# Kernel optimization log

Measured on AMD Instinct MI355X. Metric: run time of the kernel, lower is better.

## Reference

```python
import jax, jax.numpy as jnp
import numpy as np

NUM_EXPERTS = 3
INPUT_DIM = 1024
HIDDEN_DIM = 4096
OUTPUT_DIM = 1024
ROUTER_HIDDEN = 128
BATCH = 8192


def setup_inputs() -> dict:
    key = jax.random.key(0)
    ks = jax.random.split(key, 6)
    s_in = 1.0 / np.sqrt(INPUT_DIM)
    s_h = 1.0 / np.sqrt(HIDDEN_DIM)
    s_rh = 1.0 / np.sqrt(ROUTER_HIDDEN)
    return {
        "x": jax.random.normal(ks[0], (BATCH, INPUT_DIM), jnp.float32),
        "router_w1": jax.random.normal(ks[1], (INPUT_DIM, ROUTER_HIDDEN), jnp.float32) * s_in,
        "router_b1": jnp.zeros((ROUTER_HIDDEN,), jnp.float32),
        "router_w2": jax.random.normal(ks[2], (ROUTER_HIDDEN, NUM_EXPERTS), jnp.float32) * s_rh,
        "router_b2": jnp.zeros((NUM_EXPERTS,), jnp.float32),
        "expert_w1": jax.random.normal(ks[3], (NUM_EXPERTS, INPUT_DIM, HIDDEN_DIM), jnp.float32) * s_in,
        "expert_b1": jnp.zeros((NUM_EXPERTS, HIDDEN_DIM), jnp.float32),
        "expert_w2": jax.random.normal(ks[4], (NUM_EXPERTS, HIDDEN_DIM, OUTPUT_DIM), jnp.float32) * s_h,
        "expert_b2": jnp.zeros((NUM_EXPERTS, OUTPUT_DIM), jnp.float32),
    }


def reference(x, router_w1, router_b1, router_w2, router_b2,
              expert_w1, expert_b1, expert_w2, expert_b2):
    # Router: MLP -> softmax probs, hard top-1 selection (argmax)
    rh = jax.nn.relu(x @ router_w1 + router_b1)          # [B, 128]
    logits = rh @ router_w2 + router_b2                   # [B, E]
    probs = jax.nn.softmax(logits, axis=-1)
    selected = jnp.argmax(probs, axis=-1)                 # [B] int

    # Per-expert forward on all tokens (dense equivalent of masked dispatch)
    h = jax.nn.relu(jnp.einsum('bi,eih->ebh', x, expert_w1) + expert_b1[:, None, :])  # [E,B,H]
    y = jnp.einsum('ebh,eho->ebo', h, expert_w2) + expert_b2[:, None, :]              # [E,B,O]

    # Scatter-combine: each token takes its selected expert's output
    outputs = jnp.take_along_axis(
        y, selected[None, :, None], axis=0)[0]            # [B, O]

    # routing_stats: tokens per expert
    routing_stats = jnp.bincount(selected, length=NUM_EXPERTS)
    return outputs, routing_stats
```

## Files before the change

### kernel.cpp

```cpp
#include <hip/hip_runtime.h>
#include <hip/hip_bf16.h>

typedef short bf16x8 __attribute__((ext_vector_type(8)));
typedef float f32x4 __attribute__((ext_vector_type(4)));
typedef __attribute__((address_space(1))) const void gconst_t;
typedef __attribute__((address_space(3))) void lds_t;

#define DEVI __device__ __forceinline__

constexpr int BATCH   = 8192;
constexpr int IN_DIM  = 1024;
constexpr int HID     = 4096;
constexpr int OUT_DIM = 1024;
constexpr int NE      = 3;

constexpr size_t XBF_OFF  = 0;
constexpr size_t W1T_OFF  = 16777216;
constexpr size_t W2T_OFF  = W1T_OFF + 25165824;
constexpr size_t H_OFF    = W2T_OFF + 25165824;
constexpr size_t XLO_OFF  = H_OFF;
constexpr size_t RHP_OFF  = H_OFF + 16777216;
constexpr size_t META_OFF = H_OFF + 67108864;
constexpr size_t W3_OFF   = META_OFF + 131072;

DEVI unsigned short f2bf(float f) {
  __hip_bfloat16 h = __float2bfloat16(f);
  return *reinterpret_cast<unsigned short*>(&h);
}
DEVI float bf2f(unsigned short u) {
  unsigned v = (unsigned)u << 16;
  return __uint_as_float(v);
}

DEVI unsigned swz(unsigned b) { return b ^ (((b >> 7) & 7u) << 4); }

__global__ __launch_bounds__(256) void prepA_kernel(
    const float* __restrict__ x, const float* __restrict__ rw1,
    unsigned short* __restrict__ xb, unsigned short* __restrict__ xlo,
    unsigned short* __restrict__ w3) {
  __shared__ float tile[64][65];
  const int b = blockIdx.x;
  const int tid = threadIdx.x;
  if (b < 512) {
    const float4* xv4 = (const float4*)x;
    const int total = BATCH * IN_DIM / 4;
    for (int i = b * 256 + tid; i < total; i += 512 * 256) {
      const float4 v = xv4[i];
      ushort4 h, l;
      h.x = f2bf(v.x); l.x = f2bf(v.x - bf2f(h.x));
      h.y = f2bf(v.y); l.y = f2bf(v.y - bf2f(h.y));
      h.z = f2bf(v.z); l.z = f2bf(v.z - bf2f(h.z));
      h.w = f2bf(v.w); l.w = f2bf(v.w - bf2f(h.w));
      ((ushort4*)xb)[i] = h;
      ((ushort4*)xlo)[i] = l;
    }
  } else {
    const int w = b - 512;
    const int r0 = (w >> 1) * 64;
    const int c0 = (w & 1) * 64;
    const int tr = tid >> 4;
    const int tc = (tid & 15) << 2;
#pragma unroll
    for (int i = 0; i < 4; i++) {
      const int r = tr + i * 16;
      const float4 v = *(const float4*)(rw1 + (size_t)(r0 + r) * 128 + (c0 + tc));
      tile[r][tc + 0] = v.x; tile[r][tc + 1] = v.y; tile[r][tc + 2] = v.z; tile[r][tc + 3] = v.w;
    }
    __syncthreads();
#pragma unroll
    for (int i = 0; i < 4; i++) {
      const int c = tr + i * 16;
      ushort4 hi, lo;
      {
        float f;
        f = tile[tc + 0][c]; hi.x = f2bf(f); lo.x = f2bf(f - bf2f(hi.x));
        f = tile[tc + 1][c]; hi.y = f2bf(f); lo.y = f2bf(f - bf2f(hi.y));
        f = tile[tc + 2][c]; hi.z = f2bf(f); lo.z = f2bf(f - bf2f(hi.z));
        f = tile[tc + 3][c]; hi.w = f2bf(f); lo.w = f2bf(f - bf2f(hi.w));
      }
      unsigned short* base = w3 + (size_t)(c0 + c) * 3072 + (r0 + tc);
      *(ushort4*)(base)        = hi;
      *(ushort4*)(base + 1024) = hi;
      *(ushort4*)(base + 2048) = lo;
    }
  }
}

__global__ __launch_bounds__(256) void router_part(
    const unsigned short* __restrict__ xhi, const unsigned short* __restrict__ xlo,
    const unsigned short* __restrict__ w3, float* __restrict__ rhpart) {
  __shared__ unsigned short At[128 * 64];
  __shared__ unsigned short Bt[128 * 64];
  const int tid = threadIdx.x;
  const int m0 = blockIdx.x * 128;
  const int seg = blockIdx.y;
  const unsigned short* Abase = (seg == 1) ? xlo : xhi;
  const int kcol0 = seg * 1024;

  const unsigned short* asrc[4];
  const unsigned short* bsrc[4];
  unsigned loff[4];
#pragma unroll
  for (int l = 0; l < 4; l++) {
    const unsigned o = l * 4096u + (unsigned)tid * 16u;
    const unsigned p = swz(o);
    const int row = (int)(o >> 7);
    const int kel = (int)((p & 127u) >> 1);
    loff[l] = o;
    asrc[l] = Abase + (size_t)(m0 + row) * 1024 + kel;
    bsrc[l] = w3 + (size_t)row * 3072 + kcol0 + kel;
  }

  f32x4 acc[4][4];
#pragma unroll
  for (int i = 0; i < 4; i++)
#pragma unroll
    for (int j = 0; j < 4; j++) acc[i][j] = {0.f, 0.f, 0.f, 0.f};

  const int lane = tid & 63;
  const int wave = tid >> 6;
  const int wm = (wave >> 1) * 64;
  const int wn = (wave & 1) * 64;
  const int fr = lane & 15;
  const int fc = lane >> 4;

  for (int t = 0; t < 16; ++t) {
    __syncthreads();
#pragma unroll
    for (int l = 0; l < 4; l++) {
      __builtin_amdgcn_global_load_lds((gconst_t*)(asrc[l] + t * 64),
                                       (lds_t*)((char*)At + loff[l]), 16, 0, 0);
      __builtin_amdgcn_global_load_lds((gconst_t*)(bsrc[l] + t * 64),
                                       (lds_t*)((char*)Bt + loff[l]), 16, 0, 0);
    }
    __syncthreads();
    bf16x8 af[2][4], bv[2][4];
#pragma unroll
    for (int ks = 0; ks < 2; ks++) {
#pragma unroll
      for (int m = 0; m < 4; m++) {
        const unsigned L = (unsigned)(wm + m * 16 + fr) * 128u + (unsigned)(ks * 64 + fc * 16);
        af[ks][m] = *(const bf16x8*)((const char*)At + swz(L));
      }
#pragma unroll
      for (int n = 0; n < 4; n++) {
        const unsigned L = (unsigned)(wn + n * 16 + fr) * 128u + (unsigned)(ks * 64 + fc * 16);
        bv[ks][n] = *(const bf16x8*)((const char*)Bt + swz(L));
      }
    }
#pragma unroll
    for (int ks = 0; ks < 2; ks++)
#pragma unroll
      for (int m = 0; m < 4; m++)
#pragma unroll
        for (int n = 0; n < 4; n++)
          acc[m][n] = __builtin_amdgcn_mfma_f32_16x16x32_bf16(af[ks][m], bv[ks][n], acc[m][n], 0, 0, 0);
  }

  const int crow = (lane >> 4) * 4;
  const int ccol = lane & 15;
  float* outp = rhpart + (size_t)seg * BATCH * 128;
#pragma unroll
  for (int mi = 0; mi < 4; mi++) {
#pragma unroll
    for (int r = 0; r < 4; r++) {
      const int tok = m0 + wm + mi * 16 + crow + r;
#pragma unroll
      for (int ni = 0; ni < 4; ni++)
        outp[(size_t)tok * 128 + (wn + ni * 16 + ccol)] = acc[mi][ni][r];
    }
  }
}

__global__ __launch_bounds__(256) void router_finish(
    const float* __restrict__ rhpart, const float* __restrict__ rb1,
    const float* __restrict__ rw2, const float* __restrict__ rb2,
    int* __restrict__ counts, int* __restrict__ toklist) {
  __shared__ float rh[128 * 132];
  __shared__ float lg[128 * 3];
  const int tid = threadIdx.x;
  const int t0 = blockIdx.x * 128;
  constexpr size_t SEG = (size_t)BATCH * 128;

  for (int i = tid; i < 128 * 32; i += 256) {
    const int tok = i >> 5;
    const int c4 = (i & 31) * 4;
    const size_t base = (size_t)(t0 + tok) * 128 + c4;
    const float4 a = *(const float4*)(rhpart + base);
    const float4 b = *(const float4*)(rhpart + SEG + base);
    const float4 c = *(const float4*)(rhpart + 2 * SEG + base);
    const float4 bb = *(const float4*)(rb1 + c4);
    rh[tok * 132 + c4 + 0] = fmaxf(a.x + b.x + c.x + bb.x, 0.f);
    rh[tok * 132 + c4 + 1] = fmaxf(a.y + b.y + c.y + bb.y, 0.f);
    rh[tok * 132 + c4 + 2] = fmaxf(a.z + b.z + c.z + bb.z, 0.f);
    rh[tok * 132 + c4 + 3] = fmaxf(a.w + b.w + c.w + bb.w, 0.f);
  }
  __syncthreads();
#pragma unroll
  for (int pass = 0; pass < 2; ++pass) {
    const int t = tid + pass * 256;
    if (t < 384) {
      const int tok = t / 3, e = t - tok * 3;
      float s = rb2[e];
#pragma unroll 4
      for (int j = 0; j < 128; ++j) s = fmaf(rh[tok * 132 + j], rw2[j * 3 + e], s);
      lg[tok * 3 + e] = s;
    }
  }
  __syncthreads();
  if (tid < 128) {
    const float l0 = lg[tid * 3], l1 = lg[tid * 3 + 1], l2 = lg[tid * 3 + 2];
    int sel = 0; float m = l0;
    if (l1 > m) { m = l1; sel = 1; }
    if (l2 > m) { m = l2; sel = 2; }
    const int slot = atomicAdd(&counts[sel], 1);
    toklist[sel * BATCH + slot] = t0 + tid;
  }
}

__global__ __launch_bounds__(256) void prep2_kernel(
    const float* __restrict__ ew1, const float* __restrict__ ew2,
    unsigned short* __restrict__ w1t, unsigned short* __restrict__ w2t) {
  __shared__ float tile[64][65];
  const int b = blockIdx.x;
  const int tid = threadIdx.x;

  const float* src; unsigned short* dst; int R, C, r0, c0;
  if (b < 3072) {
    const int e = b / 1024, w = b % 1024;
    src = ew1 + (size_t)e * 1024 * 4096; dst = w1t + (size_t)e * 4096 * 1024;
    R = 1024; C = 4096; r0 = (w & 15) * 64; c0 = (w >> 4) * 64;
  } else {
    const int bb = b - 3072, e = bb / 1024, w = bb % 1024;
    src = ew2 + (size_t)e * 4096 * 1024; dst = w2t + (size_t)e * 1024 * 4096;
    R = 4096; C = 1024; r0 = (w & 63) * 64; c0 = (w >> 6) * 64;
  }
  const int tr = tid >> 4;
  const int tc = (tid & 15) << 2;
#pragma unroll
  for (int i = 0; i < 4; i++) {
    const int r = tr + i * 16;
    const float4 v = *(const float4*)(src + (size_t)(r0 + r) * C + (c0 + tc));
    tile[r][tc + 0] = v.x; tile[r][tc + 1] = v.y; tile[r][tc + 2] = v.z; tile[r][tc + 3] = v.w;
  }
  __syncthreads();
#pragma unroll
  for (int i = 0; i < 4; i++) {
    const int c = tr + i * 16;
    ushort4 o;
    o.x = f2bf(tile[tc + 0][c]);
    o.y = f2bf(tile[tc + 1][c]);
    o.z = f2bf(tile[tc + 2][c]);
    o.w = f2bf(tile[tc + 3][c]);
    *(ushort4*)(dst + (size_t)(c0 + c) * R + (r0 + tc)) = o;
  }
}

template <int MODE>
__global__ __launch_bounds__(512, 2) void moe_gemm(
    const unsigned short* __restrict__ Abase, const unsigned short* __restrict__ Ball,
    const float* __restrict__ biasAll, unsigned short* __restrict__ Hout,
    float* __restrict__ Yout, const int* __restrict__ toklist, const int* __restrict__ counts,
    float* __restrict__ tail) {
  constexpr int N  = (MODE == 0) ? HID : OUT_DIM;
  constexpr int K  = (MODE == 0) ? IN_DIM : HID;
  constexpr int NT = K / 32;

  const int tid = threadIdx.x;
  if (MODE == 0 && blockIdx.x == 0 && blockIdx.y == 0 && tid < NE)
    tail[tid] = (float)counts[tid];

  const int c0 = counts[0], c1 = counts[1], c2 = counts[2];
  const int mb0 = (c0 + 127) >> 7, mb1 = (c1 + 127) >> 7, mb2 = (c2 + 127) >> 7;
  const int bx = blockIdx.x;
  int e, mblk;
  if (bx < mb0) { e = 0; mblk = bx; }
  else if (bx < mb0 + mb1) { e = 1; mblk = bx - mb0; }
  else if (bx < mb0 + mb1 + mb2) { e = 2; mblk = bx - mb0 - mb1; }
  else return;
  const int cnt = (e == 0) ? c0 : (e == 1) ? c1 : c2;
  const int m0 = mblk * 128;
  const int n0 = blockIdx.y * 256;
  const int off_e = (e > 0 ? c0 : 0) + (e > 1 ? c1 : 0);
  const unsigned short* Bmat = Ball + (size_t)e * ((size_t)N * K);
  const float* bias = biasAll + (size_t)e * N;

  __shared__ unsigned short Ab[3][128 * 32];
  __shared__ unsigned short Bb[3][256 * 32];

  const unsigned short* asrc;
  const unsigned short* bsrc[2];
  unsigned aoff, boff[2];
  {
    const unsigned o = (unsigned)tid * 16u;
    const unsigned p = o ^ (((o >> 6) & 3u) << 4);
    const int row = (int)(o >> 6);
    const int kel = (int)((p & 63u) >> 1);
    aoff = o;
    int slot = m0 + row; if (slot > cnt - 1) slot = cnt - 1;
    const size_t arow = (MODE == 0) ? (size_t)toklist[e * BATCH + slot]
                                    : (size_t)(off_e + slot);
    asrc = Abase + arow * K + kel;
  }
#pragma unroll
  for (int l = 0; l < 2; l++) {
    const unsigned o = l * 8192u + (unsigned)tid * 16u;
    const unsigned p = o ^ (((o >> 6) & 3u) << 4);
    const int row = (int)(o >> 6);
    const int kel = (int)((p & 63u) >> 1);
    boff[l] = o;
    bsrc[l] = Bmat + (size_t)(n0 + row) * K + kel;
  }

  f32x4 acc[4][4];
#pragma unroll
  for (int i = 0; i < 4; i++)
#pragma unroll
    for (int j = 0; j < 4; j++) acc[i][j] = {0.f, 0.f, 0.f, 0.f};

  const int lane = tid & 63;
  const int wave = tid >> 6;
  const int wm = (wave >> 2) * 64;
  const int wn = (wave & 3) * 64;
  const int fr = lane & 15;
  const int fc = lane >> 4;

  auto STAGE = [&](int buf, int kofs) {
    __builtin_amdgcn_global_load_lds((gconst_t*)(asrc + kofs),
                                     (lds_t*)((char*)&Ab[buf][0] + aoff), 16, 0, 0);
#pragma unroll
    for (int l = 0; l < 2; l++)
      __builtin_amdgcn_global_load_lds((gconst_t*)(bsrc[l] + kofs),
                                       (lds_t*)((char*)&Bb[buf][0] + boff[l]), 16, 0, 0);
  };

  STAGE(0, 0);
  STAGE(1, 32);

  int cur = 0;
  for (int t = 0; t < NT; ++t) {
    if (t + 1 < NT) asm volatile("s_waitcnt vmcnt(3)" ::: "memory");
    else            asm volatile("s_waitcnt vmcnt(0)" ::: "memory");
    __builtin_amdgcn_sched_barrier(0);
    __builtin_amdgcn_s_barrier();
    __builtin_amdgcn_sched_barrier(0);
    bf16x8 af[4], bv[4];
#pragma unroll
    for (int m = 0; m < 4; m++) {
      const unsigned row = (unsigned)(wm + m * 16 + fr);
      const unsigned addr = ((row << 6) + (unsigned)(fc << 4)) ^ ((row & 3u) << 4);
      af[m] = *(const bf16x8*)((const char*)&Ab[cur][0] + addr);
    }
#pragma unroll
    for (int n = 0; n < 4; n++) {
      const unsigned row = (unsigned)(wn + n * 16 + fr);
      const unsigned addr = ((row << 6) + (unsigned)(fc << 4)) ^ ((row & 3u) << 4);
      bv[n] = *(const bf16x8*)((const char*)&Bb[cur][0] + addr);
    }
    asm volatile("s_waitcnt lgkmcnt(0)" ::: "memory");
    __builtin_amdgcn_sched_barrier(0);
    __builtin_amdgcn_s_setprio(1);
#pragma unroll
    for (int m = 0; m < 4; m++)
#pragma unroll
      for (int n = 0; n < 4; n++)
        acc[m][n] = __builtin_amdgcn_mfma_f32_16x16x32_bf16(af[m], bv[n], acc[m][n], 0, 0, 0);
    __builtin_amdgcn_s_setprio(0);
    if (t + 2 < NT) {
      const int nb = (cur + 2 >= 3) ? cur - 1 : cur + 2;
      STAGE(nb, (t + 2) * 32);
    }
    cur = (cur + 1 == 3) ? 0 : cur + 1;
  }

  const int crow = (lane >> 4) * 4;
  const int ccol = lane & 15;
#pragma unroll
  for (int mi = 0; mi < 4; mi++) {
#pragma unroll
    for (int r = 0; r < 4; r++) {
      const int slot = m0 + wm + mi * 16 + crow + r;
      if (slot >= cnt) continue;
      if (MODE == 0) {
        unsigned short* hrow = Hout + (size_t)(off_e + slot) * HID;
#pragma unroll
        for (int ni = 0; ni < 4; ni++) {
          const int n = n0 + wn + ni * 16 + ccol;
          const float v = acc[mi][ni][r] + bias[n];
          hrow[n] = f2bf(fmaxf(v, 0.f));
        }
      } else {
        const int tok = toklist[e * BATCH + slot];
        float* yrow = Yout + (size_t)tok * OUT_DIM;
#pragma unroll
        for (int ni = 0; ni < 4; ni++) {
          const int n = n0 + wn + ni * 16 + ccol;
          yrow[n] = acc[mi][ni][r] + bias[n];
        }
      }
    }
  }
}

extern "C" void kernel_launch(void* const* d_in, const int* in_sizes, int n_in,
                              void* d_out, int out_size, void* d_ws, size_t ws_size,
                              hipStream_t stream) {
  const float* x   = (const float*)d_in[0];
  const float* rw1 = (const float*)d_in[1];
  const float* rb1 = (const float*)d_in[2];
  const float* rw2 = (const float*)d_in[3];
  const float* rb2 = (const float*)d_in[4];
  const float* ew1 = (const float*)d_in[5];
  const float* eb1 = (const float*)d_in[6];
  const float* ew2 = (const float*)d_in[7];
  const float* eb2 = (const float*)d_in[8];
  float* out = (float*)d_out;

  char* ws = (char*)d_ws;
  unsigned short* xb  = (unsigned short*)(ws + XBF_OFF);
  unsigned short* w1t = (unsigned short*)(ws + W1T_OFF);
  unsigned short* w2t = (unsigned short*)(ws + W2T_OFF);
  unsigned short* h   = (unsigned short*)(ws + H_OFF);
  unsigned short* xlo = (unsigned short*)(ws + XLO_OFF);
  float* rhpart = (float*)(ws + RHP_OFF);
  int* counts  = (int*)(ws + META_OFF);
  int* toklist = counts + 16;
  unsigned short* w3 = (unsigned short*)(ws + W3_OFF);
  float* tail = out + (size_t)BATCH * OUT_DIM;

  hipMemsetAsync(counts, 0, 64, stream);
  prepA_kernel<<<544, 256, 0, stream>>>(x, rw1, xb, xlo, w3);
  router_part<<<dim3(64, 3), 256, 0, stream>>>(xb, xlo, w3, rhpart);
  router_finish<<<64, 256, 0, stream>>>(rhpart, rb1, rw2, rb2, counts, toklist);
  prep2_kernel<<<6144, 256, 0, stream>>>(ew1, ew2, w1t, w2t);
  moe_gemm<0><<<dim3(66, 16), 512, 0, stream>>>(xb, w1t, eb1, h, nullptr, toklist, counts, tail);
  moe_gemm<1><<<dim3(66, 4), 512, 0, stream>>>(h, w2t, eb2, nullptr, out, toklist, counts, tail);
}
```

Before: 364.0 us.

## Merge weight prep into one kernel and shrink GEMM tiles to 128x128

```diff
diff --git a/kernel.cpp b/kernel.cpp
--- a/kernel.cpp
+++ b/kernel.cpp
@@ -34,10 +34,12 @@
 
 DEVI unsigned swz(unsigned b) { return b ^ (((b >> 7) & 7u) << 4); }
 
-__global__ __launch_bounds__(256) void prepA_kernel(
+__global__ __launch_bounds__(256) void prep_all(
     const float* __restrict__ x, const float* __restrict__ rw1,
+    const float* __restrict__ ew1, const float* __restrict__ ew2,
     unsigned short* __restrict__ xb, unsigned short* __restrict__ xlo,
-    unsigned short* __restrict__ w3) {
+    unsigned short* __restrict__ w3, unsigned short* __restrict__ w1t,
+    unsigned short* __restrict__ w2t) {
   __shared__ float tile[64][65];
   const int b = blockIdx.x;
   const int tid = threadIdx.x;
@@ -54,7 +56,7 @@
       ((ushort4*)xb)[i] = h;
       ((ushort4*)xlo)[i] = l;
     }
-  } else {
+  } else if (b < 544) {
     const int w = b - 512;
     const int r0 = (w >> 1) * 64;
     const int c0 = (w & 1) * 64;
@@ -83,6 +85,37 @@
       *(ushort4*)(base + 1024) = hi;
       *(ushort4*)(base + 2048) = lo;
     }
+  } else {
+    const int bb = b - 544;
+    const float* src; unsigned short* dst; int R, C, r0, c0;
+    if (bb < 3072) {
+      const int e = bb / 1024, w = bb % 1024;
+      src = ew1 + (size_t)e * 1024 * 4096; dst = w1t + (size_t)e * 4096 * 1024;
+      R = 1024; C = 4096; r0 = (w & 15) * 64; c0 = (w >> 4) * 64;
+    } else {
+      const int b2 = bb - 3072, e = b2 / 1024, w = b2 % 1024;
+      src = ew2 + (size_t)e * 4096 * 1024; dst = w2t + (size_t)e * 1024 * 4096;
+      R = 4096; C = 1024; r0 = (w & 63) * 64; c0 = (w >> 6) * 64;
+    }
+    const int tr = tid >> 4;
+    const int tc = (tid & 15) << 2;
+#pragma unroll
+    for (int i = 0; i < 4; i++) {
+      const int r = tr + i * 16;
+      const float4 v = *(const float4*)(src + (size_t)(r0 + r) * C + (c0 + tc));
+      tile[r][tc + 0] = v.x; tile[r][tc + 1] = v.y; tile[r][tc + 2] = v.z; tile[r][tc + 3] = v.w;
+    }
+    __syncthreads();
+#pragma unroll
+    for (int i = 0; i < 4; i++) {
+      const int c = tr + i * 16;
+      ushort4 o;
+      o.x = f2bf(tile[tc + 0][c]);
+      o.y = f2bf(tile[tc + 1][c]);
+      o.z = f2bf(tile[tc + 2][c]);
+      o.w = f2bf(tile[tc + 3][c]);
+      *(ushort4*)(dst + (size_t)(c0 + c) * R + (r0 + tc)) = o;
+    }
   }
 }
 
@@ -218,46 +251,8 @@
   }
 }
 
-__global__ __launch_bounds__(256) void prep2_kernel(
-    const float* __restrict__ ew1, const float* __restrict__ ew2,
-    unsigned short* __restrict__ w1t, unsigned short* __restrict__ w2t) {
-  __shared__ float tile[64][65];
-  const int b = blockIdx.x;
-  const int tid = threadIdx.x;
-
-  const float* src; unsigned short* dst; int R, C, r0, c0;
-  if (b < 3072) {
-    const int e = b / 1024, w = b % 1024;
-    src = ew1 + (size_t)e * 1024 * 4096; dst = w1t + (size_t)e * 4096 * 1024;
-    R = 1024; C = 4096; r0 = (w & 15) * 64; c0 = (w >> 4) * 64;
-  } else {
-    const int bb = b - 3072, e = bb / 1024, w = bb % 1024;
-    src = ew2 + (size_t)e * 4096 * 1024; dst = w2t + (size_t)e * 1024 * 4096;
-    R = 4096; C = 1024; r0 = (w & 63) * 64; c0 = (w >> 6) * 64;
-  }
-  const int tr = tid >> 4;
-  const int tc = (tid & 15) << 2;
-#pragma unroll
-  for (int i = 0; i < 4; i++) {
-    const int r = tr + i * 16;
-    const float4 v = *(const float4*)(src + (size_t)(r0 + r) * C + (c0 + tc));
-    tile[r][tc + 0] = v.x; tile[r][tc + 1] = v.y; tile[r][tc + 2] = v.z; tile[r][tc + 3] = v.w;
-  }
-  __syncthreads();
-#pragma unroll
-  for (int i = 0; i < 4; i++) {
-    const int c = tr + i * 16;
-    ushort4 o;
-    o.x = f2bf(tile[tc + 0][c]);
-    o.y = f2bf(tile[tc + 1][c]);
-    o.z = f2bf(tile[tc + 2][c]);
-    o.w = f2bf(tile[tc + 3][c]);
-    *(ushort4*)(dst + (size_t)(c0 + c) * R + (r0 + tc)) = o;
-  }
-}
-
 template <int MODE>
-__global__ __launch_bounds__(512, 2) void moe_gemm(
+__global__ __launch_bounds__(256, 3) void moe_gemm(
     const unsigned short* __restrict__ Abase, const unsigned short* __restrict__ Ball,
     const float* __restrict__ biasAll, unsigned short* __restrict__ Hout,
     float* __restrict__ Yout, const int* __restrict__ toklist, const int* __restrict__ counts,
@@ -280,35 +275,29 @@
   else return;
   const int cnt = (e == 0) ? c0 : (e == 1) ? c1 : c2;
   const int m0 = mblk * 128;
-  const int n0 = blockIdx.y * 256;
+  const int n0 = blockIdx.y * 128;
   const int off_e = (e > 0 ? c0 : 0) + (e > 1 ? c1 : 0);
   const unsigned short* Bmat = Ball + (size_t)e * ((size_t)N * K);
   const float* bias = biasAll + (size_t)e * N;
 
   __shared__ unsigned short Ab[3][128 * 32];
-  __shared__ unsigned short Bb[3][256 * 32];
-
-  const unsigned short* asrc;
+  __shared__ unsigned short Bb[3][128 * 32];
+
+  const unsigned short* asrc[2];
   const unsigned short* bsrc[2];
-  unsigned aoff, boff[2];
-  {
-    const unsigned o = (unsigned)tid * 16u;
+  unsigned aoff[2], boff[2];
+#pragma unroll
+  for (int l = 0; l < 2; l++) {
+    const unsigned o = l * 4096u + (unsigned)tid * 16u;
     const unsigned p = o ^ (((o >> 6) & 3u) << 4);
     const int row = (int)(o >> 6);
     const int kel = (int)((p & 63u) >> 1);
-    aoff = o;
+    aoff[l] = o;
+    boff[l] = o;
     int slot = m0 + row; if (slot > cnt - 1) slot = cnt - 1;
     const size_t arow = (MODE == 0) ? (size_t)toklist[e * BATCH + slot]
                                     : (size_t)(off_e + slot);
-    asrc = Abase + arow * K + kel;
-  }
-#pragma unroll
-  for (int l = 0; l < 2; l++) {
-    const unsigned o = l * 8192u + (unsigned)tid * 16u;
-    const unsigned p = o ^ (((o >> 6) & 3u) << 4);
-    const int row = (int)(o >> 6);
-    const int kel = (int)((p & 63u) >> 1);
-    boff[l] = o;
+    asrc[l] = Abase + arow * K + kel;
     bsrc[l] = Bmat + (size_t)(n0 + row) * K + kel;
   }
 
@@ -320,14 +309,16 @@
 
   const int lane = tid & 63;
   const int wave = tid >> 6;
-  const int wm = (wave >> 2) * 64;
-  const int wn = (wave & 3) * 64;
+  const int wm = (wave >> 1) * 64;
+  const int wn = (wave & 1) * 64;
   const int fr = lane & 15;
   const int fc = lane >> 4;
 
   auto STAGE = [&](int buf, int kofs) {
-    __builtin_amdgcn_global_load_lds((gconst_t*)(asrc + kofs),
-                                     (lds_t*)((char*)&Ab[buf][0] + aoff), 16, 0, 0);
+#pragma unroll
+    for (int l = 0; l < 2; l++)
+      __builtin_amdgcn_global_load_lds((gconst_t*)(asrc[l] + kofs),
+                                       (lds_t*)((char*)&Ab[buf][0] + aoff[l]), 16, 0, 0);
 #pragma unroll
     for (int l = 0; l < 2; l++)
       __builtin_amdgcn_global_load_lds((gconst_t*)(bsrc[l] + kofs),
@@ -339,7 +330,7 @@
 
   int cur = 0;
   for (int t = 0; t < NT; ++t) {
-    if (t + 1 < NT) asm volatile("s_waitcnt vmcnt(3)" ::: "memory");
+    if (t + 1 < NT) asm volatile("s_waitcnt vmcnt(4)" ::: "memory");
     else            asm volatile("s_waitcnt vmcnt(0)" ::: "memory");
     __builtin_amdgcn_sched_barrier(0);
     __builtin_amdgcn_s_barrier();
@@ -429,10 +420,9 @@
   float* tail = out + (size_t)BATCH * OUT_DIM;
 
   hipMemsetAsync(counts, 0, 64, stream);
-  prepA_kernel<<<544, 256, 0, stream>>>(x, rw1, xb, xlo, w3);
+  prep_all<<<6688, 256, 0, stream>>>(x, rw1, ew1, ew2, xb, xlo, w3, w1t, w2t);
   router_part<<<dim3(64, 3), 256, 0, stream>>>(xb, xlo, w3, rhpart);
   router_finish<<<64, 256, 0, stream>>>(rhpart, rb1, rw2, rb2, counts, toklist);
-  prep2_kernel<<<6144, 256, 0, stream>>>(ew1, ew2, w1t, w2t);
-  moe_gemm<0><<<dim3(66, 16), 512, 0, stream>>>(xb, w1t, eb1, h, nullptr, toklist, counts, tail);
-  moe_gemm<1><<<dim3(66, 4), 512, 0, stream>>>(h, w2t, eb2, nullptr, out, toklist, counts, tail);
-}
+  moe_gemm<0><<<dim3(66, 32), 256, 0, stream>>>(xb, w1t, eb1, h, nullptr, toklist, counts, tail);
+  moe_gemm<1><<<dim3(66, 8), 256, 0, stream>>>(h, w2t, eb2, nullptr, out, toklist, counts, tail);
+}
```

After: 371.8 us. 1.02x slower.
